# Optimization experiments

Measured on AMD Instinct MI355X. Metric: run time of the kernel, lower is better.

## Reference

```python
import jax, jax.numpy as jnp
import numpy as np

D_MODEL = 1024
NUM_HEAD = 16


def setup_inputs() -> dict:
    key = jax.random.key(0)
    ks = jax.random.split(key, 11)
    B, S, D = 2, 2048, D_MODEL
    scale = 1.0 / np.sqrt(D)
    inp = {
        "Q": jax.random.normal(ks[0], (B, S, D), jnp.float32),
        "K": jax.random.normal(ks[1], (B, S, D), jnp.float32),
        "V": jax.random.normal(ks[2], (B, S, D), jnp.float32),
        "Wq": jax.random.normal(ks[3], (D, D), jnp.float32) * scale,
        "bq": jax.random.normal(ks[4], (D,), jnp.float32) * 0.01,
        "Wk": jax.random.normal(ks[5], (D, D), jnp.float32) * scale,
        "bk": jax.random.normal(ks[6], (D,), jnp.float32) * 0.01,
        "Wv": jax.random.normal(ks[7], (D, D), jnp.float32) * scale,
        "bv": jax.random.normal(ks[8], (D,), jnp.float32) * 0.01,
        "Wo": jax.random.normal(ks[9], (D, D), jnp.float32) * scale,
        "bo": jax.random.normal(ks[10], (D,), jnp.float32) * 0.01,
    }
    return inp


def reference(Q, K, V, Wq, bq, Wk, bk, Wv, bv, Wo, bo):
    b, vc, d_model = Q.shape
    h = NUM_HEAD
    hd = d_model // h
    # projections (torch Linear: x @ W.T + b)
    q = (Q @ Wq.T + bq).reshape(b, vc, h, hd)
    k = (K @ Wk.T + bk).reshape(b, vc, h, hd)
    v = (V @ Wv.T + bv).reshape(b, vc, h, hd)
    # scores [b,h,q,k]
    atten = jnp.einsum('bqhd,bkhd->bhqk', q, k) / np.sqrt(hd).astype(jnp.float32)
    atten = jax.nn.softmax(atten, axis=3)
    # weighted values -> [b,q,h,hd]
    out = jnp.einsum('bhqd,bdhv->bqhv', atten, v).reshape(b, vc, d_model)
    return out @ Wo.T + bo
```

## Files before the change

### kernel.cpp

```cpp
#include <hip/hip_runtime.h>

#define S_LEN 2048
#define DM 1024
#define NH 16
#define HD 64
#define NB 2

typedef unsigned short u16;
typedef __attribute__((ext_vector_type(8))) short s16x8;
typedef __attribute__((ext_vector_type(8))) unsigned short u16x8;
typedef __attribute__((ext_vector_type(4))) float fx4;
typedef __attribute__((ext_vector_type(2))) unsigned u32x2;
typedef __attribute__((ext_vector_type(4))) unsigned u32x4;

__device__ __forceinline__ u16 f2bf(float f) {
  unsigned u = __builtin_bit_cast(unsigned, f);
  return (u16)((u + 0x7FFFu + ((u >> 16) & 1u)) >> 16);
}

__device__ __forceinline__ unsigned cvt_pk_bf16(float a, float b) {
  unsigned r;
  asm("v_cvt_pk_bf16_f32 %0, %1, %2" : "=v"(r) : "v"(a), "v"(b));
  return r;
}

__device__ __forceinline__ void gload16(const void* g, void* l) {
  __builtin_amdgcn_global_load_lds(
      (const __attribute__((address_space(1))) unsigned*)g,
      (__attribute__((address_space(3))) unsigned*)l, 16, 0, 0);
}

__device__ __forceinline__ fx4 mfma16(s16x8 a, s16x8 b, fx4 c) {
  return __builtin_amdgcn_mfma_f32_16x16x32_bf16(a, b, c, 0, 0, 0);
}

__global__ __launch_bounds__(256) void cvt_all_kernel(
    const float* __restrict__ Q, const float* __restrict__ K,
    const float* __restrict__ V, const float* __restrict__ Wq,
    const float* __restrict__ Wk, const float* __restrict__ Wv,
    const float* __restrict__ Wo, u16* __restrict__ Qc, u16* __restrict__ Kc,
    u16* __restrict__ Vc, u16* __restrict__ Wqb, u16* __restrict__ Wkb,
    u16* __restrict__ Wvb, u16* __restrict__ Wob) {
  const int blk = blockIdx.x;
  const float* src;
  u16* dst;
  float scale = 1.0f;
  int off;
  if (blk < 2048)      { src = Q;  dst = Qc;  off = blk; }
  else if (blk < 4096) { src = K;  dst = Kc;  off = blk - 2048; }
  else if (blk < 6144) { src = V;  dst = Vc;  off = blk - 4096; }
  else if (blk < 6656) { src = Wq; dst = Wqb; off = blk - 6144; scale = 0.18033688f; }
  else if (blk < 7168) { src = Wk; dst = Wkb; off = blk - 6656; }
  else if (blk < 7680) { src = Wv; dst = Wvb; off = blk - 7168; }
  else                 { src = Wo; dst = Wob; off = blk - 7680; }
  const int i = (off * 256 + (int)threadIdx.x) * 8;
  fx4 a = *(const fx4*)(src + i);
  fx4 b = *(const fx4*)(src + i + 4);
  u16x8 o;
  o[0] = f2bf(a[0] * scale); o[1] = f2bf(a[1] * scale);
  o[2] = f2bf(a[2] * scale); o[3] = f2bf(a[3] * scale);
  o[4] = f2bf(b[0] * scale); o[5] = f2bf(b[1] * scale);
  o[6] = f2bf(b[2] * scale); o[7] = f2bf(b[3] * scale);
  *(u16x8*)(dst + i) = o;
}

__device__ __forceinline__ void store_out(u16* C, size_t idx, float v) { C[idx] = f2bf(v); }
__device__ __forceinline__ void store_out(float* C, size_t idx, float v) { C[idx] = v; }

template <typename OUT>
__device__ __forceinline__ void gemm_pipe_body(const u16* __restrict__ A,
                                               const u16* __restrict__ Bt,
                                               const float* __restrict__ bias,
                                               float bscale, OUT* __restrict__ C,
                                               u16* __restrict__ vt, bool vout,
                                               int m0, int n0) {
  __shared__ u16 Al[3][128 * 32];
  __shared__ u16 Bl[3][128 * 32];
  const int tid = threadIdx.x;
  const int wid = tid >> 6, lane = tid & 63;
  const int g = lane >> 4, lr = lane & 15;
  const int wr = wid >> 1, wc = wid & 1;
  const int row0 = tid >> 2, ch = tid & 3;
  const int chx = ch ^ ((row0 >> 1) & 3);

  fx4 acc[4][4] = {};

  auto stage = [&](u16* Ab, u16* Bb, int k0) {
    gload16(A + (size_t)(m0 + row0) * 1024 + k0 + chx * 8, (char*)Ab + wid * 1024);
    gload16(A + (size_t)(m0 + 64 + row0) * 1024 + k0 + chx * 8,
            (char*)Ab + 4096 + wid * 1024);
    gload16(Bt + (size_t)(n0 + row0) * 1024 + k0 + chx * 8, (char*)Bb + wid * 1024);
    gload16(Bt + (size_t)(n0 + 64 + row0) * 1024 + k0 + chx * 8,
            (char*)Bb + 4096 + wid * 1024);
  };
  auto readfrag = [&](const u16* Ab, const u16* Bb, s16x8* a, s16x8* b) {
#pragma unroll
    for (int m = 0; m < 4; ++m) {
      const int row = wr * 64 + m * 16 + lr;
      a[m] = *(const s16x8*)((const char*)Ab + row * 64 + (g ^ ((row >> 1) & 3)) * 16);
    }
#pragma unroll
    for (int n = 0; n < 4; ++n) {
      const int row = wc * 64 + n * 16 + lr;
      b[n] = *(const s16x8*)((const char*)Bb + row * 64 + (g ^ ((row >> 1) & 3)) * 16);
    }
  };
  auto domfma = [&](s16x8* a, s16x8* b) {
    __builtin_amdgcn_s_setprio(1);
#pragma unroll
    for (int m = 0; m < 4; ++m)
#pragma unroll
      for (int n = 0; n < 4; ++n) acc[m][n] = mfma16(a[m], b[n], acc[m][n]);
    __builtin_amdgcn_s_setprio(0);
  };

#define GSTEP(BUF, T, NW)                                                     \
  do {                                                                        \
    asm volatile("s_waitcnt vmcnt(" #NW ")" ::: "memory");                    \
    __builtin_amdgcn_s_barrier();                                             \
    __builtin_amdgcn_sched_barrier(0);                                        \
    s16x8 afr[4], bfr[4];                                                     \
    readfrag(Al[BUF], Bl[BUF], afr, bfr);                                     \
    asm volatile("s_waitcnt lgkmcnt(0)" ::: "memory");                        \
    __builtin_amdgcn_sched_barrier(0);                                        \
    __builtin_amdgcn_s_barrier();                                             \
    __builtin_amdgcn_sched_barrier(0);                                        \
    if ((T) + 3 < 32) stage(Al[BUF], Bl[BUF], ((T) + 3) * 32);                \
    domfma(afr, bfr);                                                         \
  } while (0)

  stage(Al[0], Bl[0], 0);
  stage(Al[1], Bl[1], 32);
  stage(Al[2], Bl[2], 64);

#pragma unroll 1
  for (int t = 0; t < 30; t += 3) {
    GSTEP(0, t, 8);
    GSTEP(1, t + 1, 8);
    GSTEP(2, t + 2, 8);
  }
  GSTEP(0, 30, 4);
  GSTEP(1, 31, 0);
#undef GSTEP

  if (vout) {
#pragma unroll
    for (int n = 0; n < 4; ++n) {
      const int col = n0 + wc * 64 + n * 16 + lr;
      const float bv = bias[col] * bscale;
      const int h = col >> 6, d = col & 63;
#pragma unroll
      for (int m = 0; m < 4; ++m) {
        const int row = m0 + wr * 64 + m * 16 + g * 4;
        const int bb = row >> 11, s = row & 2047;
        u32x2 w;
        w[0] = cvt_pk_bf16(acc[m][n][0] + bv, acc[m][n][1] + bv);
        w[1] = cvt_pk_bf16(acc[m][n][2] + bv, acc[m][n][3] + bv);
        *(u32x2*)(vt + ((size_t)(((bb << 4) | h) * 64 + d)) * 2048 + s) = w;
      }
    }
  } else {
#pragma unroll
    for (int n = 0; n < 4; ++n) {
      const int col = n0 + wc * 64 + n * 16 + lr;
      const float bv = bias[col] * bscale;
#pragma unroll
      for (int m = 0; m < 4; ++m) {
        const int row = m0 + wr * 64 + m * 16 + g * 4;
#pragma unroll
        for (int j = 0; j < 4; ++j)
          store_out(C, (size_t)(row + j) * 1024 + col, acc[m][n][j] + bv);
      }
    }
  }
}

__global__ __launch_bounds__(256, 3) void gemm_qkv_kernel(
    const u16* Qc, const u16* Kc, const u16* Vc, const u16* Wq, const u16* Wk,
    const u16* Wv, const float* bq, const float* bk, const float* bv, u16* q,
    u16* k, u16* vt) {
  const int hw = blockIdx.x + (blockIdx.y << 3) + (blockIdx.z << 8);
  const int xcd = hw & 7, j = hw >> 3;
  const int x = j & 7;
  const int p = xcd + ((j >> 3) << 3);
  const int y = p & 31, z = p >> 5;

  const u16 *Ap, *Bp;
  const float* bp;
  u16* Cp;
  float bs = 1.0f;
  bool vo = false;
  if (z == 0)      { Ap = Qc; Bp = Wq; bp = bq; Cp = q; bs = 0.18033688f; }
  else if (z == 1) { Ap = Kc; Bp = Wk; bp = bk; Cp = k; }
  else             { Ap = Vc; Bp = Wv; bp = bv; Cp = q; vo = true; }
  gemm_pipe_body<u16>(Ap, Bp, bp, bs, Cp, vt, vo, y * 128, x * 128);
}

__global__ __launch_bounds__(256, 3) void gemm_out_kernel(const u16* ctx,
                                                          const u16* Wo,
                                                          const float* bo,
                                                          float* out) {
  const int hw = blockIdx.x + (blockIdx.y << 3);
  const int xcd = hw & 7, j = hw >> 3;
  const int x = j & 7;
  const int y = xcd + ((j >> 3) << 3);
  gemm_pipe_body<float>(ctx, Wo, bo, 1.0f, out, nullptr, false, y * 128, x * 128);
}

__global__ __launch_bounds__(256, 2) void attn_kernel(const u16* __restrict__ qb,
                                                      const u16* __restrict__ kb,
                                                      const u16* __restrict__ vt,
                                                      u16* __restrict__ ctx) {
  __shared__ u16 Kl[2][64 * 64];
  __shared__ u16 Vl[2][64 * 64];
  __shared__ u16 Pl[4][32 * 64];

  const int tid = threadIdx.x, wid = tid >> 6, lane = tid & 63;
  const int g = lane >> 4, lr = lane & 15;
  const int rswz = (lr & 7) * 8;
  const int pswz = (lr & 7) * 16;
  char* Pb = (char*)&Pl[wid][0];

  const int hw = blockIdx.x;
  const int xcd = hw & 7, slot = hw >> 3;
  const int bh = xcd * 4 + (slot >> 4);
  const int b = bh >> 4, h = bh & 15;
  const int q0 = (slot & 15) * 128;

  const u16* qp = qb + ((size_t)(b * S_LEN + q0 + wid * 32 + lr)) * DM + h * HD;
  s16x8 aq0[2], aq1[2];
  aq0[0] = *(const s16x8*)(qp + g * 8);
  aq0[1] = *(const s16x8*)(qp + 32 + g * 8);
  aq1[0] = *(const s16x8*)(qp + (size_t)16 * DM + g * 8);
  aq1[1] = *(const s16x8*)(qp + (size_t)16 * DM + 32 + g * 8);

  fx4 accO0[4] = {}, accO1[4] = {};
  float lrun0 = 0.f, lrun1 = 0.f;

  const int srow = tid >> 3, sch = tid & 7;
  const int schx = sch ^ (srow & 7);
  const u16* kbase = kb + ((size_t)b * S_LEN) * DM + h * HD;
  const u16* vtbase = vt + ((size_t)bh * 64) * S_LEN;

#define STAGE(buf, kv)                                                             \
  do {                                                                             \
    gload16(kbase + (size_t)((kv) + srow) * DM + schx * 8,                         \
            (char*)Kl[buf] + wid * 1024);                                          \
    gload16(kbase + (size_t)((kv) + 32 + srow) * DM + schx * 8,                    \
            (char*)Kl[buf] + 4096 + wid * 1024);                                   \
    gload16(vtbase + (size_t)srow * S_LEN + (kv) + schx * 8,                       \
            (char*)Vl[buf] + wid * 1024);                                          \
    gload16(vtbase + (size_t)(32 + srow) * S_LEN + (kv) + schx * 8,                \
            (char*)Vl[buf] + 4096 + wid * 1024);                                   \
  } while (0)

#define ASTEP(BUF, T, NW)                                                          \
  do {                                                                             \
    asm volatile("s_waitcnt vmcnt(" #NW ")" ::: "memory");                         \
    __builtin_amdgcn_s_barrier();                                                  \
    __builtin_amdgcn_sched_barrier(0);                                             \
    fx4 s0[4] = {}, s1[4] = {};                                                    \
    s16x8 vf0[4], vf1[4];                                                          \
    __builtin_amdgcn_s_setprio(1);                                                 \
    _Pragma("unroll") for (int ks = 0; ks < 2; ++ks) {                             \
      _Pragma("unroll") for (int c = 0; c < 4; ++c) {                              \
        s16x8 kf = *(const s16x8*)(Kl[BUF] + (c * 16 + lr) * 64 +                  \
                                   ((ks * 32 + g * 8) ^ rswz));                    \
        s0[c] = mfma16(kf, ks ? aq0[1] : aq0[0], s0[c]);                           \
        s1[c] = mfma16(kf, ks ? aq1[1] : aq1[0], s1[c]);                           \
      }                                                                            \
    }                                                                              \
    __builtin_amdgcn_s_setprio(0);                                                 \
    _Pragma("unroll") for (int c = 0; c < 4; ++c) {                                \
      vf0[c] = *(const s16x8*)(Vl[BUF] + (c * 16 + lr) * 64 + ((g * 8) ^ rswz));   \
      vf1[c] =                                                                     \
          *(const s16x8*)(Vl[BUF] + (c * 16 + lr) * 64 + ((32 + g * 8) ^ rswz));   \
    }                                                                              \
    asm volatile("s_waitcnt lgkmcnt(0)" ::: "memory");                             \
    __builtin_amdgcn_sched_barrier(0);                                             \
    __builtin_amdgcn_s_barrier();                                                  \
    __builtin_amdgcn_sched_barrier(0);                                             \
    if ((T) + 2 < 32) STAGE(BUF, ((T) + 2) * 64);                                  \
      \
    _Pragma("unroll") for (int c = 0; c < 4; ++c)                                  \
        _Pragma("unroll") for (int j = 0; j < 4; ++j) {                            \
      s0[c][j] = __builtin_amdgcn_exp2f(s0[c][j]);                                 \
      s1[c][j] = __builtin_amdgcn_exp2f(s1[c][j]);                                 \
    }                                                                              \
    lrun0 += ((s0[0][0] + s0[0][1]) + (s0[0][2] + s0[0][3])) +                     \
             ((s0[1][0] + s0[1][1]) + (s0[1][2] + s0[1][3])) +                     \
             ((s0[2][0] + s0[2][1]) + (s0[2][2] + s0[2][3])) +                     \
             ((s0[3][0] + s0[3][1]) + (s0[3][2] + s0[3][3]));                      \
    lrun1 += ((s1[0][0] + s1[0][1]) + (s1[0][2] + s1[0][3])) +                     \
             ((s1[1][0] + s1[1][1]) + (s1[1][2] + s1[1][3])) +                     \
             ((s1[2][0] + s1[2][1]) + (s1[2][2] + s1[2][3])) +                     \
             ((s1[3][0] + s1[3][1]) + (s1[3][2] + s1[3][3]));                      \
                     \
    _Pragma("unroll") for (int c = 0; c < 4; ++c) {                                \
      u32x2 w0, w1;                                                                \
      w0[0] = cvt_pk_bf16(s0[c][0], s0[c][1]);                                     \
      w0[1] = cvt_pk_bf16(s0[c][2], s0[c][3]);                                     \
      w1[0] = cvt_pk_bf16(s1[c][0], s1[c][1]);                                     \
      w1[1] = cvt_pk_bf16(s1[c][2], s1[c][3]);                                     \
      *(u32x2*)(Pb + lr * 128 + ((c * 32 + g * 8) ^ pswz)) = w0;                   \
      *(u32x2*)(Pb + (16 + lr) * 128 + ((c * 32 + g * 8) ^ pswz)) = w1;            \
    }                                                                              \
                                         \
    __builtin_amdgcn_s_setprio(1);                                                 \
    {                                                                              \
      s16x8 pb00 = *(const s16x8*)(Pb + lr * 128 + ((g * 16) ^ pswz));             \
      s16x8 pb01 = *(const s16x8*)(Pb + lr * 128 + ((64 + g * 16) ^ pswz));        \
      s16x8 pb10 = *(const s16x8*)(Pb + (16 + lr) * 128 + ((g * 16) ^ pswz));      \
      s16x8 pb11 =                                                                 \
          *(const s16x8*)(Pb + (16 + lr) * 128 + ((64 + g * 16) ^ pswz));          \
      _Pragma("unroll") for (int c = 0; c < 4; ++c) {                              \
        accO0[c] = mfma16(vf0[c], pb00, accO0[c]);                                 \
        accO0[c] = mfma16(vf1[c], pb01, accO0[c]);                                 \
        accO1[c] = mfma16(vf0[c], pb10, accO1[c]);                                 \
        accO1[c] = mfma16(vf1[c], pb11, accO1[c]);                                 \
      }                                                                            \
    }                                                                              \
    __builtin_amdgcn_s_setprio(0);                                                 \
  } while (0)

  STAGE(0, 0);
  STAGE(1, 64);

#pragma unroll 1
  for (int t = 0; t < 30; t += 2) {
    ASTEP(0, t, 4);
    ASTEP(1, t + 1, 4);
  }
  ASTEP(0, 30, 4);
  ASTEP(1, 31, 0);
#undef ASTEP
#undef STAGE

  lrun0 += __shfl_xor(lrun0, 16);
  lrun0 += __shfl_xor(lrun0, 32);
  lrun1 += __shfl_xor(lrun1, 16);
  lrun1 += __shfl_xor(lrun1, 32);
  const float inv0 = 1.0f / lrun0;
  const float inv1 = 1.0f / lrun1;
  u16* op0 = ctx + ((size_t)(b * S_LEN + q0 + wid * 32 + lr)) * DM + h * HD;
  u16* op1 = op0 + (size_t)16 * DM;
#pragma unroll
  for (int c = 0; c < 4; ++c) {
    u32x2 w0, w1;
    w0[0] = cvt_pk_bf16(accO0[c][0] * inv0, accO0[c][1] * inv0);
    w0[1] = cvt_pk_bf16(accO0[c][2] * inv0, accO0[c][3] * inv0);
    w1[0] = cvt_pk_bf16(accO1[c][0] * inv1, accO1[c][1] * inv1);
    w1[1] = cvt_pk_bf16(accO1[c][2] * inv1, accO1[c][3] * inv1);
    *(u32x2*)(op0 + c * 16 + g * 4) = w0;
    *(u32x2*)(op1 + c * 16 + g * 4) = w1;
  }
}

extern "C" void kernel_launch(void* const* d_in, const int* in_sizes, int n_in,
                              void* d_out, int out_size, void* d_ws, size_t ws_size,
                              hipStream_t stream) {
  const float* Q = (const float*)d_in[0];
  const float* K = (const float*)d_in[1];
  const float* V = (const float*)d_in[2];
  const float* Wq = (const float*)d_in[3];
  const float* bq = (const float*)d_in[4];
  const float* Wk = (const float*)d_in[5];
  const float* bk = (const float*)d_in[6];
  const float* Wv = (const float*)d_in[7];
  const float* bv = (const float*)d_in[8];
  const float* Wo = (const float*)d_in[9];
  const float* bo = (const float*)d_in[10];
  float* out = (float*)d_out;

  char* ws = (char*)d_ws;
  const size_t SZ_T = (size_t)NB * S_LEN * DM * 2;
  const size_t SZ_W = (size_t)DM * DM * 2;

  u16* Wqb = (u16*)(ws);
  u16* Wkb = (u16*)(ws + SZ_W);
  u16* Wvb = (u16*)(ws + 2 * SZ_W);
  u16* Wob = (u16*)(ws + 3 * SZ_W);
  u16* Qc  = (u16*)(ws + 4 * SZ_W);
  u16* Kc  = (u16*)(ws + 4 * SZ_W + SZ_T);
  u16* Vc  = (u16*)(ws + 4 * SZ_W + 2 * SZ_T);
  u16* qb  = (u16*)(ws + 4 * SZ_W + 3 * SZ_T);
  u16* kb  = (u16*)(ws + 4 * SZ_W + 4 * SZ_T);
  u16* vtb = (u16*)(ws + 4 * SZ_W + 5 * SZ_T);
  u16* ctx = Qc;

  cvt_all_kernel<<<8192, 256, 0, stream>>>(Q, K, V, Wq, Wk, Wv, Wo, Qc, Kc, Vc,
                                           Wqb, Wkb, Wvb, Wob);

  gemm_qkv_kernel<<<dim3(8, 32, 3), 256, 0, stream>>>(Qc, Kc, Vc, Wqb, Wkb, Wvb,
                                                      bq, bk, bv, qb, kb, vtb);

  attn_kernel<<<512, 256, 0, stream>>>(qb, kb, vtb, ctx);

  gemm_out_kernel<<<dim3(8, 32), 256, 0, stream>>>(ctx, Wob, bo, out);
}
```

Measured before the change: 111.0 us.

## Fuse fp32-to-bf16 activation conversion into QKV GEMM loads

The fp32 Q/K/V activations are no longer converted to bf16 by a separate pass. The QKV GEMM now streams fp32 tiles directly into LDS with a new swizzle and converts them to bf16 while reading fragments, and the conversion kernel only handles the weights. This removes a full read/write round trip of the activations plus the bf16 staging buffers. In exchange the GEMM reads twice as many A bytes per tile, its LDS pipeline drops from triple to double buffering, and the output GEMM gets its own specialised copy of the old body.

```diff
diff --git a/kernel.cpp b/kernel.cpp
--- a/kernel.cpp
+++ b/kernel.cpp
@@ -34,25 +34,20 @@
   return __builtin_amdgcn_mfma_f32_16x16x32_bf16(a, b, c, 0, 0, 0);
 }
 
-__global__ __launch_bounds__(256) void cvt_all_kernel(
-    const float* __restrict__ Q, const float* __restrict__ K,
-    const float* __restrict__ V, const float* __restrict__ Wq,
-    const float* __restrict__ Wk, const float* __restrict__ Wv,
-    const float* __restrict__ Wo, u16* __restrict__ Qc, u16* __restrict__ Kc,
-    u16* __restrict__ Vc, u16* __restrict__ Wqb, u16* __restrict__ Wkb,
-    u16* __restrict__ Wvb, u16* __restrict__ Wob) {
+__global__ __launch_bounds__(256) void cvt_w_kernel(
+    const float* __restrict__ Wq, const float* __restrict__ Wk,
+    const float* __restrict__ Wv, const float* __restrict__ Wo,
+    u16* __restrict__ Wqb, u16* __restrict__ Wkb, u16* __restrict__ Wvb,
+    u16* __restrict__ Wob) {
   const int blk = blockIdx.x;
   const float* src;
   u16* dst;
   float scale = 1.0f;
   int off;
-  if (blk < 2048)      { src = Q;  dst = Qc;  off = blk; }
-  else if (blk < 4096) { src = K;  dst = Kc;  off = blk - 2048; }
-  else if (blk < 6144) { src = V;  dst = Vc;  off = blk - 4096; }
-  else if (blk < 6656) { src = Wq; dst = Wqb; off = blk - 6144; scale = 0.18033688f; }
-  else if (blk < 7168) { src = Wk; dst = Wkb; off = blk - 6656; }
-  else if (blk < 7680) { src = Wv; dst = Wvb; off = blk - 7168; }
-  else                 { src = Wo; dst = Wob; off = blk - 7680; }
+  if (blk < 512)       { src = Wq; dst = Wqb; off = blk;        scale = 0.18033688f; }
+  else if (blk < 1024) { src = Wk; dst = Wkb; off = blk - 512;  }
+  else if (blk < 1536) { src = Wv; dst = Wvb; off = blk - 1024; }
+  else                 { src = Wo; dst = Wob; off = blk - 1536; }
   const int i = (off * 256 + (int)threadIdx.x) * 8;
   fx4 a = *(const fx4*)(src + i);
   fx4 b = *(const fx4*)(src + i + 4);
@@ -67,81 +62,83 @@
 __device__ __forceinline__ void store_out(u16* C, size_t idx, float v) { C[idx] = f2bf(v); }
 __device__ __forceinline__ void store_out(float* C, size_t idx, float v) { C[idx] = v; }
 
-template <typename OUT>
-__device__ __forceinline__ void gemm_pipe_body(const u16* __restrict__ A,
-                                               const u16* __restrict__ Bt,
-                                               const float* __restrict__ bias,
-                                               float bscale, OUT* __restrict__ C,
-                                               u16* __restrict__ vt, bool vout,
-                                               int m0, int n0) {
-  __shared__ u16 Al[3][128 * 32];
-  __shared__ u16 Bl[3][128 * 32];
+__device__ __forceinline__ void gemm_f32_pipe(const float* __restrict__ Afp,
+                                              const u16* __restrict__ Bt,
+                                              const float* __restrict__ bias,
+                                              float bscale, u16* __restrict__ C,
+                                              u16* __restrict__ vt, bool vout,
+                                              int m0, int n0) {
+  __shared__ u16 Al[2][128 * 64];
+  __shared__ u16 Bl[2][128 * 32];
   const int tid = threadIdx.x;
   const int wid = tid >> 6, lane = tid & 63;
   const int g = lane >> 4, lr = lane & 15;
   const int wr = wid >> 1, wc = wid & 1;
   const int row0 = tid >> 2, ch = tid & 3;
   const int chx = ch ^ ((row0 >> 1) & 3);
+  const int arow = tid >> 3;
+  const int acs = (tid & 7) ^ (arow & 7);
 
   fx4 acc[4][4] = {};
 
-  auto stage = [&](u16* Ab, u16* Bb, int k0) {
-    gload16(A + (size_t)(m0 + row0) * 1024 + k0 + chx * 8, (char*)Ab + wid * 1024);
-    gload16(A + (size_t)(m0 + 64 + row0) * 1024 + k0 + chx * 8,
-            (char*)Ab + 4096 + wid * 1024);
-    gload16(Bt + (size_t)(n0 + row0) * 1024 + k0 + chx * 8, (char*)Bb + wid * 1024);
+  auto stage = [&](int buf, int k0) {
+#pragma unroll
+    for (int p = 0; p < 4; ++p)
+      gload16(Afp + (size_t)(m0 + p * 32 + arow) * 1024 + k0 + acs * 4,
+              (char*)Al[buf] + p * 4096 + wid * 1024);
+    gload16(Bt + (size_t)(n0 + row0) * 1024 + k0 + chx * 8,
+            (char*)Bl[buf] + wid * 1024);
     gload16(Bt + (size_t)(n0 + 64 + row0) * 1024 + k0 + chx * 8,
-            (char*)Bb + 4096 + wid * 1024);
+            (char*)Bl[buf] + 4096 + wid * 1024);
   };
-  auto readfrag = [&](const u16* Ab, const u16* Bb, s16x8* a, s16x8* b) {
-#pragma unroll
-    for (int m = 0; m < 4; ++m) {
-      const int row = wr * 64 + m * 16 + lr;
-      a[m] = *(const s16x8*)((const char*)Ab + row * 64 + (g ^ ((row >> 1) & 3)) * 16);
-    }
-#pragma unroll
-    for (int n = 0; n < 4; ++n) {
-      const int row = wc * 64 + n * 16 + lr;
-      b[n] = *(const s16x8*)((const char*)Bb + row * 64 + (g ^ ((row >> 1) & 3)) * 16);
-    }
-  };
-  auto domfma = [&](s16x8* a, s16x8* b) {
-    __builtin_amdgcn_s_setprio(1);
-#pragma unroll
-    for (int m = 0; m < 4; ++m)
-#pragma unroll
-      for (int n = 0; n < 4; ++n) acc[m][n] = mfma16(a[m], b[n], acc[m][n]);
-    __builtin_amdgcn_s_setprio(0);
-  };
-
-#define GSTEP(BUF, T, NW)                                                     \
-  do {                                                                        \
-    asm volatile("s_waitcnt vmcnt(" #NW ")" ::: "memory");                    \
-    __builtin_amdgcn_s_barrier();                                             \
-    __builtin_amdgcn_sched_barrier(0);                                        \
-    s16x8 afr[4], bfr[4];                                                     \
-    readfrag(Al[BUF], Bl[BUF], afr, bfr);                                     \
-    asm volatile("s_waitcnt lgkmcnt(0)" ::: "memory");                        \
-    __builtin_amdgcn_sched_barrier(0);                                        \
-    __builtin_amdgcn_s_barrier();                                             \
-    __builtin_amdgcn_sched_barrier(0);                                        \
-    if ((T) + 3 < 32) stage(Al[BUF], Bl[BUF], ((T) + 3) * 32);                \
-    domfma(afr, bfr);                                                         \
+
+#define QSTEP(BUF, T, NW)                                                     \
+  do {                                                                       \
+    asm volatile("s_waitcnt vmcnt(" #NW ")" ::: "memory");                   \
+    __builtin_amdgcn_s_barrier();                                            \
+    __builtin_amdgcn_sched_barrier(0);                                       \
+    s16x8 afr[4], bfr[4];                                                    \
+    _Pragma("unroll") for (int m = 0; m < 4; ++m) {                          \
+      const int row = wr * 64 + m * 16 + lr;                                 \
+      fx4 x = *(const fx4*)((const char*)Al[BUF] + row * 128 +               \
+                            ((2 * g) ^ (lr & 7)) * 16);                      \
+      fx4 y = *(const fx4*)((const char*)Al[BUF] + row * 128 +               \
+                            ((2 * g + 1) ^ (lr & 7)) * 16);                  \
+      u32x4 w;                                                               \
+      w[0] = cvt_pk_bf16(x[0], x[1]);                                        \
+      w[1] = cvt_pk_bf16(x[2], x[3]);                                        \
+      w[2] = cvt_pk_bf16(y[0], y[1]);                                        \
+      w[3] = cvt_pk_bf16(y[2], y[3]);                                        \
+      afr[m] = __builtin_bit_cast(s16x8, w);                                 \
+    }                                                                        \
+    _Pragma("unroll") for (int n = 0; n < 4; ++n) {                          \
+      const int row = wc * 64 + n * 16 + lr;                                 \
+      bfr[n] = *(const s16x8*)((const char*)Bl[BUF] + row * 64 +             \
+                               (g ^ ((row >> 1) & 3)) * 16);                 \
+    }                                                                        \
+    asm volatile("s_waitcnt lgkmcnt(0)" ::: "memory");                       \
+    __builtin_amdgcn_sched_barrier(0);                                       \
+    __builtin_amdgcn_s_barrier();                                            \
+    __builtin_amdgcn_sched_barrier(0);                                       \
+    if ((T) + 2 < 32) stage(BUF, ((T) + 2) * 32);                            \
+    __builtin_amdgcn_s_setprio(1);                                           \
+    _Pragma("unroll") for (int m = 0; m < 4; ++m)                            \
+        _Pragma("unroll") for (int n = 0; n < 4; ++n) acc[m][n] =            \
+        mfma16(afr[m], bfr[n], acc[m][n]);                                   \
+    __builtin_amdgcn_s_setprio(0);                                           \
   } while (0)
 
-  stage(Al[0], Bl[0], 0);
-  stage(Al[1], Bl[1], 32);
-  stage(Al[2], Bl[2], 64);
+  stage(0, 0);
+  stage(1, 32);
 
 #pragma unroll 1
-  for (int t = 0; t < 30; t += 3) {
-    GSTEP(0, t, 8);
-    GSTEP(1, t + 1, 8);
-    GSTEP(2, t + 2, 8);
-  }
-  GSTEP(0, 30, 4);
-  GSTEP(1, 31, 0);
-#undef GSTEP
+  for (int t = 0; t < 30; t += 2) {
+    QSTEP(0, t, 6);
+    QSTEP(1, t + 1, 6);
+  }
+  QSTEP(0, 30, 6);
+  QSTEP(1, 31, 0);
+#undef QSTEP
 
   if (vout) {
 #pragma unroll
@@ -176,7 +173,7 @@
 }
 
 __global__ __launch_bounds__(256, 3) void gemm_qkv_kernel(
-    const u16* Qc, const u16* Kc, const u16* Vc, const u16* Wq, const u16* Wk,
+    const float* Q, const float* K, const float* V, const u16* Wq, const u16* Wk,
     const u16* Wv, const float* bq, const float* bk, const float* bv, u16* q,
     u16* k, u16* vt) {
   const int hw = blockIdx.x + (blockIdx.y << 3) + (blockIdx.z << 8);
@@ -185,26 +182,102 @@
   const int p = xcd + ((j >> 3) << 3);
   const int y = p & 31, z = p >> 5;
 
-  const u16 *Ap, *Bp;
+  const float* Ap;
+  const u16* Bp;
   const float* bp;
   u16* Cp;
   float bs = 1.0f;
   bool vo = false;
-  if (z == 0)      { Ap = Qc; Bp = Wq; bp = bq; Cp = q; bs = 0.18033688f; }
-  else if (z == 1) { Ap = Kc; Bp = Wk; bp = bk; Cp = k; }
-  else             { Ap = Vc; Bp = Wv; bp = bv; Cp = q; vo = true; }
-  gemm_pipe_body<u16>(Ap, Bp, bp, bs, Cp, vt, vo, y * 128, x * 128);
-}
-
-__global__ __launch_bounds__(256, 3) void gemm_out_kernel(const u16* ctx,
-                                                          const u16* Wo,
-                                                          const float* bo,
-                                                          float* out) {
+  if (z == 0)      { Ap = Q; Bp = Wq; bp = bq; Cp = q; bs = 0.18033688f; }
+  else if (z == 1) { Ap = K; Bp = Wk; bp = bk; Cp = k; }
+  else             { Ap = V; Bp = Wv; bp = bv; Cp = q; vo = true; }
+  gemm_f32_pipe(Ap, Bp, bp, bs, Cp, vt, vo, y * 128, x * 128);
+}
+
+__global__ __launch_bounds__(256, 3) void gemm_out_kernel(const u16* __restrict__ ctx,
+                                                          const u16* __restrict__ Wo,
+                                                          const float* __restrict__ bo,
+                                                          float* __restrict__ out) {
   const int hw = blockIdx.x + (blockIdx.y << 3);
   const int xcd = hw & 7, j = hw >> 3;
   const int x = j & 7;
   const int y = xcd + ((j >> 3) << 3);
-  gemm_pipe_body<float>(ctx, Wo, bo, 1.0f, out, nullptr, false, y * 128, x * 128);
+  const int m0 = y * 128, n0 = x * 128;
+
+  __shared__ u16 Al[3][128 * 32];
+  __shared__ u16 Bl[3][128 * 32];
+  const int tid = threadIdx.x;
+  const int wid = tid >> 6, lane = tid & 63;
+  const int g = lane >> 4, lr = lane & 15;
+  const int wr = wid >> 1, wc = wid & 1;
+  const int row0 = tid >> 2, ch = tid & 3;
+  const int chx = ch ^ ((row0 >> 1) & 3);
+
+  fx4 acc[4][4] = {};
+
+  auto stage = [&](u16* Ab, u16* Bb, int k0) {
+    gload16(ctx + (size_t)(m0 + row0) * 1024 + k0 + chx * 8, (char*)Ab + wid * 1024);
+    gload16(ctx + (size_t)(m0 + 64 + row0) * 1024 + k0 + chx * 8,
+            (char*)Ab + 4096 + wid * 1024);
+    gload16(Wo + (size_t)(n0 + row0) * 1024 + k0 + chx * 8, (char*)Bb + wid * 1024);
+    gload16(Wo + (size_t)(n0 + 64 + row0) * 1024 + k0 + chx * 8,
+            (char*)Bb + 4096 + wid * 1024);
+  };
+
+#define GSTEP(BUF, T, NW)                                                     \
+  do {                                                                        \
+    asm volatile("s_waitcnt vmcnt(" #NW ")" ::: "memory");                    \
+    __builtin_amdgcn_s_barrier();                                             \
+    __builtin_amdgcn_sched_barrier(0);                                        \
+    s16x8 afr[4], bfr[4];                                                     \
+    _Pragma("unroll") for (int m = 0; m < 4; ++m) {                           \
+      const int row = wr * 64 + m * 16 + lr;                                  \
+      afr[m] = *(const s16x8*)((const char*)Al[BUF] + row * 64 +              \
+                               (g ^ ((row >> 1) & 3)) * 16);                  \
+    }                                                                         \
+    _Pragma("unroll") for (int n = 0; n < 4; ++n) {                           \
+      const int row = wc * 64 + n * 16 + lr;                                  \
+      bfr[n] = *(const s16x8*)((const char*)Bl[BUF] + row * 64 +              \
+                               (g ^ ((row >> 1) & 3)) * 16);                  \
+    }                                                                         \
+    asm volatile("s_waitcnt lgkmcnt(0)" ::: "memory");                        \
+    __builtin_amdgcn_sched_barrier(0);                                        \
+    __builtin_amdgcn_s_barrier();                                             \
+    __builtin_amdgcn_sched_barrier(0);                                        \
+    if ((T) + 3 < 32) stage(Al[BUF], Bl[BUF], ((T) + 3) * 32);                \
+    __builtin_amdgcn_s_setprio(1);                                            \
+    _Pragma("unroll") for (int m = 0; m < 4; ++m)                             \
+        _Pragma("unroll") for (int n = 0; n < 4; ++n) acc[m][n] =             \
+        mfma16(afr[m], bfr[n], acc[m][n]);                                    \
+    __builtin_amdgcn_s_setprio(0);                                            \
+  } while (0)
+
+  stage(Al[0], Bl[0], 0);
+  stage(Al[1], Bl[1], 32);
+  stage(Al[2], Bl[2], 64);
+
+#pragma unroll 1
+  for (int t = 0; t < 30; t += 3) {
+    GSTEP(0, t, 8);
+    GSTEP(1, t + 1, 8);
+    GSTEP(2, t + 2, 8);
+  }
+  GSTEP(0, 30, 4);
+  GSTEP(1, 31, 0);
+#undef GSTEP
+
+#pragma unroll
+  for (int n = 0; n < 4; ++n) {
+    const int col = n0 + wc * 64 + n * 16 + lr;
+    const float bv = bo[col];
+#pragma unroll
+    for (int m = 0; m < 4; ++m) {
+      const int row = m0 + wr * 64 + m * 16 + g * 4;
+#pragma unroll
+      for (int j = 0; j < 4; ++j)
+        out[(size_t)(row + j) * 1024 + col] = acc[m][n][j] + bv;
+    }
+  }
 }
 
 __global__ __launch_bounds__(256, 2) void attn_kernel(const u16* __restrict__ qb,
@@ -380,18 +453,14 @@
   u16* Wkb = (u16*)(ws + SZ_W);
   u16* Wvb = (u16*)(ws + 2 * SZ_W);
   u16* Wob = (u16*)(ws + 3 * SZ_W);
-  u16* Qc  = (u16*)(ws + 4 * SZ_W);
-  u16* Kc  = (u16*)(ws + 4 * SZ_W + SZ_T);
-  u16* Vc  = (u16*)(ws + 4 * SZ_W + 2 * SZ_T);
-  u16* qb  = (u16*)(ws + 4 * SZ_W + 3 * SZ_T);
-  u16* kb  = (u16*)(ws + 4 * SZ_W + 4 * SZ_T);
-  u16* vtb = (u16*)(ws + 4 * SZ_W + 5 * SZ_T);
-  u16* ctx = Qc;
-
-  cvt_all_kernel<<<8192, 256, 0, stream>>>(Q, K, V, Wq, Wk, Wv, Wo, Qc, Kc, Vc,
-                                           Wqb, Wkb, Wvb, Wob);
-
-  gemm_qkv_kernel<<<dim3(8, 32, 3), 256, 0, stream>>>(Qc, Kc, Vc, Wqb, Wkb, Wvb,
+  u16* qb  = (u16*)(ws + 4 * SZ_W);
+  u16* kb  = (u16*)(ws + 4 * SZ_W + SZ_T);
+  u16* vtb = (u16*)(ws + 4 * SZ_W + 2 * SZ_T);
+  u16* ctx = (u16*)(ws + 4 * SZ_W + 3 * SZ_T);
+
+  cvt_w_kernel<<<2048, 256, 0, stream>>>(Wq, Wk, Wv, Wo, Wqb, Wkb, Wvb, Wob);
+
+  gemm_qkv_kernel<<<dim3(8, 32, 3), 256, 0, stream>>>(Q, K, V, Wqb, Wkb, Wvb,
                                                       bq, bk, bv, qb, kb, vtb);
 
   attn_kernel<<<512, 256, 0, stream>>>(qb, kb, vtb, ctx);
```

Measured after the change: 107.5 us, median of 2. 3.1% less time.
